# Kernel tuning notes

Measured on AMD Instinct MI355X. Metric: run time of the kernel, lower is better.

## Reference

```python
import jax, jax.numpy as jnp
import numpy as np

G = 32; N = G * G          # gridsize, num_nodes per graph
A = 16                      # n_agents
B = 32                      # batch_size
E = 4096                    # edges per graph (~4-neighbor grid)
F_IN = 16                   # input_dim
H = 64                      # hidden_dim
L = 3                       # n_graph_layers
MID = F_IN + L * H          # 208
CAT = 2 * MID + H           # 480
MIN_VAL = -1e8


def _layer_norm(x, g, b, eps=1e-5):
    m = x.mean(-1, keepdims=True)
    v = x.var(-1, keepdims=True)
    return (x - m) * jax.lax.rsqrt(v + eps) * g + b


def setup_inputs() -> dict:
    key = jax.random.key(0)
    ks = jax.random.split(key, 16)
    inp = {}
    inp["graph_nodes"] = jax.random.normal(ks[0], (B, N, F_IN), jnp.float32)
    inp["graph_edge_links"] = jax.random.randint(ks[1], (B, 2, E), 0, N)
    inp["agent_locations"] = jax.random.randint(ks[2], (B, A), 0, N)
    inp["mask"] = jax.random.bernoulli(ks[3], 0.5, (B, A * N))
    inp["dist_matrix"] = jax.random.uniform(ks[4], (N, N), jnp.float32)
    dims = [F_IN] + [H] * L
    k = 5
    for l in range(L):
        inp[f"conv{l}_W"] = jax.random.normal(ks[k], (dims[l], H), jnp.float32) * 0.05
        inp[f"conv{l}_b"] = jnp.zeros((H,), jnp.float32)
        inp[f"conv{l}_g"] = jnp.ones((H,), jnp.float32)
        inp[f"conv{l}_beta"] = jnp.zeros((H,), jnp.float32)
        k += 1
    inp["edges_W"] = jax.random.normal(ks[k], (1, H), jnp.float32) * 0.05
    inp["edges_b"] = jnp.zeros((H,), jnp.float32)
    inp["actor1_W"] = jax.random.normal(ks[k + 1], (CAT, MID), jnp.float32) * 0.05
    inp["actor1_b"] = jnp.zeros((MID,), jnp.float32)
    inp["bn_g"] = jnp.ones((MID,), jnp.float32)
    inp["bn_b"] = jnp.zeros((MID,), jnp.float32)
    inp["actor2_W"] = jax.random.normal(ks[k + 2], (MID, 1), jnp.float32) * 0.05
    inp["actor2_b"] = jnp.zeros((1,), jnp.float32)
    return inp


def reference(graph_nodes, graph_edge_links, agent_locations, mask, dist_matrix,
              conv0_W, conv0_b, conv0_g, conv0_beta,
              conv1_W, conv1_b, conv1_g, conv1_beta,
              conv2_W, conv2_b, conv2_g, conv2_beta,
              edges_W, edges_b, actor1_W, actor1_b, bn_g, bn_b,
              actor2_W, actor2_b):
    # --- batch graphs: offset node indices per graph (Batch.from_data_list) ---
    x = graph_nodes.reshape(B * N, F_IN)
    offs = (jnp.arange(B) * N)[:, None, None]
    ei = (graph_edge_links + offs).transpose(1, 0, 2).reshape(2, B * E)
    src, dst = ei[0], ei[1]

    conv_params = [(conv0_W, conv0_b, conv0_g, conv0_beta),
                   (conv1_W, conv1_b, conv1_g, conv1_beta),
                   (conv2_W, conv2_b, conv2_g, conv2_beta)]
    outs = [x]
    for W, bb, g, beta in conv_params:
        # GINConv with eps=-1: (1+eps)*x_i == 0, so out = mlp(sum_j x_j)
        agg = jax.ops.segment_sum(x[src], dst, num_segments=B * N)
        x = jax.nn.relu(_layer_norm(agg @ W + bb, g, beta))  # mlp relu; outer .relu() idempotent
        outs.append(x)
    xc = jnp.concatenate(outs, axis=1).reshape(B, N, MID)

    # --- all-pairs (agent, node) feature build ---
    a = jnp.take_along_axis(xc, agent_locations[:, :, None], axis=1)  # [B, A, MID]
    a = jnp.repeat(a, N, axis=1)                                      # [B, A*N, MID]
    bfeat = jnp.tile(xc, (1, A, 1))                                   # [B, A*N, MID]
    c = dist_matrix[agent_locations].reshape(B, A * N, 1)             # [B, A*N, 1]
    c = c @ edges_W + edges_b                                         # [B, A*N, H]
    h = jnp.concatenate([a, bfeat, c], axis=2).reshape(-1, CAT)

    h = h @ actor1_W + actor1_b
    mu = h.mean(0)
    var = h.var(0)
    h = (h - mu) * jax.lax.rsqrt(var + 1e-5) * bn_g + bn_b  # BatchNorm1d, training stats
    h = jax.nn.relu(h)
    logits = (h @ actor2_W + actor2_b).reshape(B, A * N)
    logits = jnp.where(mask, logits, MIN_VAL)
    return jax.nn.softmax(logits, axis=1)
```

## Files before the change

kernel.cpp:

```cpp
#include <hip/hip_runtime.h>
#include <cstddef>

#define B_    32
#define N_    1024
#define E_    4096
#define A_    16
#define FIN_  16
#define H_    64
#define MID_  208
#define NODES (B_ * N_)
#define NEDGE (B_ * E_)
#define ROWS  (B_ * A_ * N_)
#define AN_   (A_ * N_)

__device__ __forceinline__ float readlane_f(float v, int l) {
  return __uint_as_float(__builtin_amdgcn_readlane(__float_as_uint(v), l));
}

__global__ __launch_bounds__(256) void k_front(const int* __restrict__ el,
                                               const float* __restrict__ dist,
                                               const int* __restrict__ loc,
                                               const float* __restrict__ W1,
                                               const float* __restrict__ eW,
                                               const float* __restrict__ eb,
                                               const float* __restrict__ b1,
                                               int* __restrict__ rowptr,
                                               int* __restrict__ counts,
                                               int* __restrict__ ssrc,
                                               float* __restrict__ d1row,
                                               float* __restrict__ c2row,
                                               float* __restrict__ e1,
                                               float* __restrict__ cu,
                                               float* __restrict__ base) {
  __shared__ int cnt[1024];
  __shared__ int cur[1024];
  __shared__ int part[256];
  __shared__ int loc_s[16];
  int blk = blockIdx.x, t = threadIdx.x;
  if (blk < 32) {
    int b = blk;
    for (int i = t; i < 1024; i += 256) cnt[i] = 0;
    __syncthreads();
    const int* srcp = el + b * (2 * E_);
    const int* dstp = srcp + E_;
    for (int i = t; i < E_; i += 256) atomicAdd(&cnt[dstp[i]], 1);
    __syncthreads();
    int4 c4 = *(const int4*)&cnt[t * 4];
    int s = c4.x + c4.y + c4.z + c4.w;
    part[t] = s;
    __syncthreads();
    for (int off = 1; off < 256; off <<= 1) {
      int v = (t >= off) ? part[t - off] : 0;
      __syncthreads();
      part[t] += v;
      __syncthreads();
    }
    int prev = ((t == 0) ? 0 : part[t - 1]) + b * E_;
    int p0 = prev, p1 = p0 + c4.x, p2 = p1 + c4.y, p3 = p2 + c4.z;
    *(int4*)&rowptr[b * 1024 + t * 4] = make_int4(p0, p1, p2, p3);
    *(int4*)&counts[b * 1024 + t * 4] = c4;
    cur[t * 4 + 0] = p0;
    cur[t * 4 + 1] = p1;
    cur[t * 4 + 2] = p2;
    cur[t * 4 + 3] = p3;
    __syncthreads();
    for (int i = t; i < E_; i += 256) {
      int dl = dstp[i];
      int sl = srcp[i];
      int pos = atomicAdd(&cur[dl], 1);
      ssrc[pos] = b * N_ + sl;
    }
  } else if (blk < 288) {
    int lane = t & 63, w = t >> 6;
    int r = (blk - 32) * 4 + w;
    const float* dr = dist + (size_t)r * N_;
    float s = 0.f, c2 = 0.f;
#pragma unroll
    for (int k = 0; k < 16; k++) {
      float v = dr[lane + 64 * k];
      s += v;
      c2 = fmaf(v, v, c2);
    }
#pragma unroll
    for (int o = 32; o > 0; o >>= 1) { s += __shfl_xor(s, o); c2 += __shfl_xor(c2, o); }
    if (lane == 0) { d1row[r] = s; c2row[r] = c2; }
  } else if (blk < 320) {
    int b = blk - 288;
    if (t < 16) loc_s[t] = loc[b * 16 + t];
    __syncthreads();
    float e4[4] = {0.f, 0.f, 0.f, 0.f};
    for (int a = 0; a < 16; a++) {
      const float* dr = dist + (size_t)loc_s[a] * N_;
#pragma unroll
      for (int k = 0; k < 4; k++) e4[k] += dr[t + 256 * k];
    }
#pragma unroll
    for (int k = 0; k < 4; k++) e1[b * N_ + t + 256 * k] = e4[k];
  } else {
    int j = t;
    if (j < MID_) {
      float c = 0.f, bs = 0.f;
      for (int k = 0; k < H_; k++) {
        float w = W1[(2 * MID_ + k) * MID_ + j];
        c = fmaf(eW[k], w, c);
        bs = fmaf(eb[k], w, bs);
      }
      cu[j] = c;
      base[j] = bs + b1[j];
    }
  }
}

template <int FINT, bool COPYIN>
__global__ __launch_bounds__(256) void k_layer(const float* __restrict__ xin, int xstride, int in_off,
                                               float* __restrict__ xc, int out_off,
                                               const int* __restrict__ rowptr,
                                               const int* __restrict__ counts,
                                               const int* __restrict__ ssrc,
                                               const float* __restrict__ W,
                                               const float* __restrict__ bias,
                                               const float* __restrict__ g,
                                               const float* __restrict__ beta) {
  int t = threadIdx.x, lane = t & 63, w = t >> 6;
  float Wcol[FINT];
#pragma unroll
  for (int f = 0; f < FINT; f++) Wcol[f] = W[f * 64 + lane];
  float bv = bias[lane], gv = g[lane], bev = beta[lane];
  constexpr int CH = 64 / FINT;
  int f = lane & (FINT - 1);
  int ch = (FINT == 64) ? 0 : (lane >> 4);
  int nbase = (blockIdx.x * 4 + w) * 4;

  float agg[4];
#pragma unroll
  for (int nn = 0; nn < 4; nn++) {
    int node = nbase + nn;
    int r0 = rowptr[node];
    int deg = counts[node];
    float a0 = 0.f, a1 = 0.f, a2 = 0.f, a3 = 0.f;
    int e = ch;
    for (; e + 3 * CH < deg; e += 4 * CH) {
      int s0 = ssrc[r0 + e];
      int s1 = ssrc[r0 + e + CH];
      int s2 = ssrc[r0 + e + 2 * CH];
      int s3 = ssrc[r0 + e + 3 * CH];
      a0 += xin[(size_t)s0 * xstride + in_off + f];
      a1 += xin[(size_t)s1 * xstride + in_off + f];
      a2 += xin[(size_t)s2 * xstride + in_off + f];
      a3 += xin[(size_t)s3 * xstride + in_off + f];
    }
    for (; e < deg; e += CH) {
      int s = ssrc[r0 + e];
      a0 += xin[(size_t)s * xstride + in_off + f];
    }
    agg[nn] = (a0 + a1) + (a2 + a3);
  }

#pragma unroll
  for (int nn = 0; nn < 4; nn++) {
    int node = nbase + nn;
    float aggf = agg[nn];
    float y0 = bv, y1 = 0.f, y2 = 0.f, y3 = 0.f;
#pragma unroll
    for (int l = 0; l < 64; l += 4) {
      y0 = fmaf(readlane_f(aggf, l + 0), Wcol[(l + 0) & (FINT - 1)], y0);
      y1 = fmaf(readlane_f(aggf, l + 1), Wcol[(l + 1) & (FINT - 1)], y1);
      y2 = fmaf(readlane_f(aggf, l + 2), Wcol[(l + 2) & (FINT - 1)], y2);
      y3 = fmaf(readlane_f(aggf, l + 3), Wcol[(l + 3) & (FINT - 1)], y3);
    }
    float y = (y0 + y1) + (y2 + y3);
    float m = y;
#pragma unroll
    for (int o = 32; o > 0; o >>= 1) m += __shfl_xor(m, o);
    m *= (1.f / 64.f);
    float d = y - m;
    float vv = d * d;
#pragma unroll
    for (int o = 32; o > 0; o >>= 1) vv += __shfl_xor(vv, o);
    vv *= (1.f / 64.f);
    float outv = fmaxf(d * rsqrtf(vv + 1e-5f) * gv + bev, 0.f);
    xc[(size_t)node * MID_ + out_off + lane] = outv;
    if (COPYIN) {
      if (lane < FIN_) xc[(size_t)node * MID_ + lane] = xin[(size_t)node * FIN_ + lane];
    }
  }
}

template <int NR>
__device__ __forceinline__ void gemm_sc(const float* __restrict__ xc,
                                        const float* __restrict__ W1,
                                        int row0w, int j0, float acc[NR][4]) {
  const float* Bbase = W1 + (size_t)MID_ * MID_;
  const float* Arow = xc + (size_t)row0w * MID_;
#pragma unroll
  for (int r = 0; r < NR; r++)
#pragma unroll
    for (int q = 0; q < 4; q++) acc[r][q] = 0.f;

#pragma unroll 2
  for (int c = 0; c < 52; c++) {
    int k = c * 4;
    float4 a[NR];
    const float* ap = Arow + k;
#pragma unroll
    for (int r = 0; r < NR; r++) a[r] = *(const float4*)(ap + r * MID_);
#pragma unroll
    for (int q = 0; q < 4; q++) {
      float4 bq = *(const float4*)(Bbase + (size_t)(k + q) * MID_ + j0);
#pragma unroll
      for (int r = 0; r < NR; r++) {
        float ar = (q == 0) ? a[r].x : (q == 1) ? a[r].y : (q == 2) ? a[r].z : a[r].w;
        acc[r][0] = fmaf(ar, bq.x, acc[r][0]);
        acc[r][1] = fmaf(ar, bq.y, acc[r][1]);
        acc[r][2] = fmaf(ar, bq.z, acc[r][2]);
        acc[r][3] = fmaf(ar, bq.w, acc[r][3]);
      }
    }
  }
}

#define TSTR 105
__global__ __launch_bounds__(256) void k_p1(const float* __restrict__ xc,
                                            const float* __restrict__ W1,
                                            const float* __restrict__ e1,
                                            const int* __restrict__ loc,
                                            float* __restrict__ SBp,
                                            float* __restrict__ pBT,
                                            float* __restrict__ pA) {
  __shared__ float red[4 * 624];
  __shared__ float accS[32 * TSTR];
  __shared__ float xr[MID_];
  int t = threadIdx.x, lane = t & 63;
  int w = __builtin_amdgcn_readfirstlane(t >> 6);
  int blk = blockIdx.x;
  if (blk < 1024) {
    int row0 = blk * 32;
    int row0w = row0 + w * 8;
    int j0 = lane * 4;
    float acc[8][4];
    gemm_sc<8>(xc, W1, row0w, j0, acc);
    const float* ep = e1 + row0w;
    float4 e0 = *(const float4*)(ep);
    float4 e4 = *(const float4*)(ep + 4);
    float ev[8] = {e0.x, e0.y, e0.z, e0.w, e4.x, e4.y, e4.z, e4.w};
    if (j0 < MID_) {
      float s1[4] = {0, 0, 0, 0}, s2[4] = {0, 0, 0, 0}, se[4] = {0, 0, 0, 0};
#pragma unroll
      for (int r = 0; r < 8; r++) {
#pragma unroll
        for (int q = 0; q < 4; q++) {
          float v = acc[r][q];
          s1[q] += v;
          s2[q] = fmaf(v, v, s2[q]);
          se[q] = fmaf(v, ev[r], se[q]);
        }
      }
#pragma unroll
      for (int q = 0; q < 4; q++) {
        red[w * 624 + j0 + q] = s1[q];
        red[w * 624 + 208 + j0 + q] = s2[q];
        red[w * 624 + 416 + j0 + q] = se[q];
      }
    }
    __syncthreads();
    for (int idx = t; idx < 624; idx += 256) {
      SBp[(size_t)blk * 624 + idx] =
          (red[idx] + red[624 + idx]) + (red[1248 + idx] + red[1872 + idx]);
    }
#pragma unroll
    for (int half = 0; half < 2; half++) {
      int lo = half * 104;
      __syncthreads();
      if (j0 >= lo && j0 < lo + 104) {
        int jc = j0 - lo;
#pragma unroll
        for (int r = 0; r < 8; r++) {
          int ba = (w * 8 + r) * TSTR + jc;
          accS[ba + 0] = acc[r][0];
          accS[ba + 1] = acc[r][1];
          accS[ba + 2] = acc[r][2];
          accS[ba + 3] = acc[r][3];
        }
      }
      __syncthreads();
      int jb = lo + w * 26;
      if (lane < 32) {
#pragma unroll 2
        for (int jj = 0; jj < 26; jj++) {
          int j = jb + jj;
          pBT[(size_t)j * NODES + row0 + lane] = accS[lane * TSTR + (j - lo)];
        }
      }
    }
  } else {
    int ab = blk - 1024;
    int b = ab >> 4;
    int node = b * N_ + loc[ab];
    if (t < MID_) xr[t] = xc[(size_t)node * MID_ + t];
    __syncthreads();
    if (t < MID_) {
      float acc = 0.f;
      for (int i = 0; i < MID_; i++) acc = fmaf(xr[i], W1[i * MID_ + t], acc);
      pA[ab * MID_ + t] = acc;
    }
  }
}

__global__ __launch_bounds__(256) void k_fin(const float* __restrict__ SBp,
                                             const float* __restrict__ pA,
                                             const float* __restrict__ cu,
                                             const float* __restrict__ base,
                                             const float* __restrict__ d1row,
                                             const float* __restrict__ c2row,
                                             const int* __restrict__ loc,
                                             const float* __restrict__ bng,
                                             const float* __restrict__ bnb,
                                             const float* __restrict__ W2,
                                             float* __restrict__ vaT,
                                             float* __restrict__ wpack4) {
  __shared__ float utmp[1536 + 192];
  __shared__ float redm[4];
  __shared__ float reds[4];
  __shared__ float bcast[2];
  int t = threadIdx.x, lane = t & 63, w = t >> 6;
  int j = blockIdx.x;
  float cuj = cu[j], bj = base[j];
  int bb = t >> 3, ii = t & 7;
  float q1 = 0, q2 = 0, q3 = 0, t1 = 0, t2 = 0, t3 = 0;
#pragma unroll
  for (int i = ii * 4; i < ii * 4 + 4; i++) {
    const float* sp = SBp + (size_t)(bb * 32 + i) * 624;
    q1 += sp[j];
    q2 += sp[208 + j];
    q3 += sp[416 + j];
  }
#pragma unroll
  for (int a = ii * 2; a < ii * 2 + 2; a++) {
    int r = bb * 16 + a;
    float pa = pA[r * MID_ + j] + bj;
    t1 += pa;
    t2 = fmaf(pa, pa, t2);
    t3 = fmaf(pa, d1row[loc[r]], t3);
  }
  utmp[0 * 256 + t] = q1;
  utmp[1 * 256 + t] = q2;
  utmp[2 * 256 + t] = q3;
  utmp[3 * 256 + t] = t1;
  utmp[4 * 256 + t] = t2;
  utmp[5 * 256 + t] = t3;
  float p1 = 0.f, p2 = 0.f;
#pragma unroll
  for (int r = t * 2; r < t * 2 + 2; r++) {
    int l = loc[r];
    p1 += d1row[l];
    p2 += c2row[l];
  }
#pragma unroll
  for (int o = 32; o > 0; o >>= 1) { p1 += __shfl_xor(p1, o); p2 += __shfl_xor(p2, o); }
  if (lane == 0) { redm[w] = p1; reds[w] = p2; }
  __syncthreads();
  if (t < 192) {
    int s = t >> 5, b32 = t & 31;
    float ssum = 0.f;
#pragma unroll
    for (int i = 0; i < 8; i++) ssum += utmp[s * 256 + b32 * 8 + i];
    utmp[1536 + s * 32 + b32] = ssum;
  }
  __syncthreads();
  if (t == 0) {
    float Sc1 = (redm[0] + redm[1]) + (redm[2] + redm[3]);
    float Sc2 = (reds[0] + reds[1]) + (reds[2] + reds[3]);
    double T1 = 0, T2 = 0, T3 = 0, cross = 0, sp1 = 0, sp2 = 0, spe = 0;
    for (int b = 0; b < 32; b++) {
      float sq1 = utmp[1536 + 0 * 32 + b];
      float sq2 = utmp[1536 + 1 * 32 + b];
      float sq3 = utmp[1536 + 2 * 32 + b];
      float pt1 = utmp[1536 + 3 * 32 + b];
      float pt2 = utmp[1536 + 4 * 32 + b];
      float pt3 = utmp[1536 + 5 * 32 + b];
      T1 += pt1; T2 += pt2; T3 += pt3;
      cross += (double)pt1 * sq1;
      sp1 += sq1; sp2 += sq2; spe += sq3;
    }
    double s1 = 1024.0 * T1 + 16.0 * sp1 + (double)cuj * Sc1;
    double s2 = 1024.0 * T2 + 16.0 * sp2 + (double)cuj * cuj * Sc2 +
                2.0 * (cross + (double)cuj * (T3 + spe));
    double mu = s1 * (1.0 / (double)ROWS);
    double var = s2 * (1.0 / (double)ROWS) - mu * mu;
    float sc = (float)(1.0 / sqrt(var + 1e-5)) * bng[j];
    float sh = bnb[j] - (float)mu * sc;
    bcast[0] = sc;
    bcast[1] = sh;
    wpack4[4 * j + 0] = sc;
    wpack4[4 * j + 1] = cuj * sc;
    wpack4[4 * j + 2] = W2[j];
    wpack4[4 * j + 3] = 0.f;
  }
  __syncthreads();
  float sc = bcast[0], sh = bcast[1];
#pragma unroll
  for (int r = t * 2; r < t * 2 + 2; r++) {
    int b = r >> 4, a = r & 15;
    float pa = pA[r * MID_ + j] + bj;
    vaT[((size_t)b * MID_ + j) * 16 + a] = pa * sc + sh;
  }
}

__global__ __launch_bounds__(256) void k_logits(const float* __restrict__ pBT,
                                                const float* __restrict__ vaT,
                                                const float* __restrict__ wpack4,
                                                const float* __restrict__ dist,
                                                const int* __restrict__ loc,
                                                const int* __restrict__ mask,
                                                const float* __restrict__ b2,
                                                float* __restrict__ lg,
                                                float2* __restrict__ Psm) {
  __shared__ float accL[4][8][64];
  __shared__ int loc_s[16];
  __shared__ float redm[4];
  __shared__ float reds[4];
  int t = threadIdx.x, lane = t & 63;
  int w = __builtin_amdgcn_readfirstlane(t >> 6);
  int b = blockIdx.y, nt = blockIdx.x;
  int n0 = nt * 64;
  if (t < 16) loc_s[t] = loc[b * 16 + t];
  __syncthreads();
  float c[16];
#pragma unroll
  for (int a = 0; a < 16; a++) c[a] = dist[(size_t)loc_s[a] * N_ + n0 + lane];
  float acc16[16];
#pragma unroll
  for (int a = 0; a < 16; a++) acc16[a] = 0.f;
  const float4* wp = (const float4*)wpack4;
  int ng = b * N_ + n0 + lane;
  int jb = w * 52;
#pragma unroll 4
  for (int jj = 0; jj < 52; jj++) {
    int j = jb + jj;
    float pbv = pBT[(size_t)j * NODES + ng];
    float4 wv = wp[j];
    float pbs = pbv * wv.x;
    const float* va = vaT + ((size_t)b * MID_ + j) * 16;
#pragma unroll
    for (int a = 0; a < 16; a++) {
      float h = fmaf(c[a], wv.y, va[a] + pbs);
      h = fmaxf(h, 0.f);
      acc16[a] = fmaf(h, wv.z, acc16[a]);
    }
  }

  float b2v = b2[0];
  float sv[4];
  int ois[4];
  unsigned mk = 0;
#pragma unroll
  for (int half = 0; half < 2; half++) {
#pragma unroll
    for (int a8 = 0; a8 < 8; a8++) accL[t >> 6][a8][lane] = acc16[half * 8 + a8];
    __syncthreads();
#pragma unroll
    for (int p = 0; p < 2; p++) {
      int idx = p * 256 + t;
      int a8 = idx >> 6, nn = idx & 63;
      float s = (accL[0][a8][nn] + accL[1][a8][nn]) +
                (accL[2][a8][nn] + accL[3][a8][nn]) + b2v;
      int a = half * 8 + a8;
      int oi = b * AN_ + a * N_ + n0 + nn;
      int iv = half * 2 + p;
      bool m_ = mask[oi] != 0;
      sv[iv] = m_ ? s : -1e8f;
      ois[iv] = oi;
      mk |= (m_ ? 1u : 0u) << iv;
    }
    __syncthreads();
  }

  float mx = fmaxf(fmaxf(sv[0], sv[1]), fmaxf(sv[2], sv[3]));
#pragma unroll
  for (int o = 32; o > 0; o >>= 1) mx = fmaxf(mx, __shfl_xor(mx, o));
  if (lane == 0) redm[t >> 6] = mx;
  __syncthreads();
  mx = fmaxf(fmaxf(redm[0], redm[1]), fmaxf(redm[2], redm[3]));
  float ssum = 0.f;
#pragma unroll
  for (int iv = 0; iv < 4; iv++) {
    float pv = ((mk >> iv) & 1u) ? expf(sv[iv] - mx) : 0.f;
    lg[ois[iv]] = pv;
    ssum += pv;
  }
#pragma unroll
  for (int o = 32; o > 0; o >>= 1) ssum += __shfl_xor(ssum, o);
  if (lane == 0) reds[t >> 6] = ssum;
  __syncthreads();
  if (t == 0) Psm[b * 16 + nt] = make_float2(mx, (reds[0] + reds[1]) + (reds[2] + reds[3]));
}

__global__ __launch_bounds__(256) void k_sm2(const float* __restrict__ lg,
                                             const float2* __restrict__ P,
                                             float* __restrict__ out) {
  __shared__ float scs[16];
  int b = blockIdx.y, x = blockIdx.x, t = threadIdx.x;
  float M = -3.0e38f;
  float2 pr[16];
#pragma unroll
  for (int k = 0; k < 16; k++) {
    pr[k] = P[b * 16 + k];
    M = fmaxf(M, pr[k].x);
  }
  float S = 0.f;
#pragma unroll
  for (int k = 0; k < 16; k++) S += pr[k].y * expf(pr[k].x - M);
  float inv = 1.0f / S;
  if (t < 16) scs[t] = expf(pr[t].x - M) * inv;
  __syncthreads();
  const float* lb = lg + b * AN_ + x * 2048;
  float* ob = out + b * AN_ + x * 2048;
#pragma unroll
  for (int k = 0; k < 8; k++) {
    int i = t + 256 * k;
    int n = (x * 2048 + i) & 1023;
    ob[i] = lb[i] * scs[n >> 6];
  }
}

extern "C" void kernel_launch(void* const* d_in, const int* in_sizes, int n_in,
                              void* d_out, int out_size, void* d_ws, size_t ws_size,
                              hipStream_t stream) {
  const float* gn = (const float*)d_in[0];
  const int* el = (const int*)d_in[1];
  const int* loc = (const int*)d_in[2];
  const int* mask = (const int*)d_in[3];
  const float* dist = (const float*)d_in[4];
  const float* c0W = (const float*)d_in[5];
  const float* c0b = (const float*)d_in[6];
  const float* c0g = (const float*)d_in[7];
  const float* c0be = (const float*)d_in[8];
  const float* c1W = (const float*)d_in[9];
  const float* c1b = (const float*)d_in[10];
  const float* c1g = (const float*)d_in[11];
  const float* c1be = (const float*)d_in[12];
  const float* c2W = (const float*)d_in[13];
  const float* c2b = (const float*)d_in[14];
  const float* c2g = (const float*)d_in[15];
  const float* c2be = (const float*)d_in[16];
  const float* eW = (const float*)d_in[17];
  const float* eb = (const float*)d_in[18];
  const float* W1 = (const float*)d_in[19];
  const float* b1 = (const float*)d_in[20];
  const float* bng = (const float*)d_in[21];
  const float* bnb = (const float*)d_in[22];
  const float* W2 = (const float*)d_in[23];
  const float* b2 = (const float*)d_in[24];
  float* out = (float*)d_out;

  char* p = (char*)d_ws;
  auto alloc = [&](size_t bytes) {
    char* r = p;
    p += (bytes + 255) & ~(size_t)255;
    return r;
  };
  int* counts = (int*)alloc((size_t)NODES * 4);
  int* rowptr = (int*)alloc((size_t)NODES * 4);
  int* ssrc = (int*)alloc((size_t)NEDGE * 4);
  float* xc = (float*)alloc((size_t)NODES * MID_ * 4);
  float* pBT = (float*)alloc((size_t)NODES * MID_ * 4);
  float* pA = (float*)alloc((size_t)512 * MID_ * 4);
  float* cu = (float*)alloc(256 * 4);
  float* base = (float*)alloc(256 * 4);
  float* d1row = (float*)alloc((size_t)N_ * 4);
  float* c2row = (float*)alloc((size_t)N_ * 4);
  float* e1 = (float*)alloc((size_t)B_ * N_ * 4);
  float* SBp = (float*)alloc((size_t)1024 * 624 * 4);
  float* vaT = (float*)alloc((size_t)B_ * MID_ * 16 * 4);
  float* wpack4 = (float*)alloc((size_t)MID_ * 4 * 4);
  float* lg = (float*)alloc((size_t)ROWS * 4);
  float2* Psm = (float2*)alloc((size_t)B_ * 16 * 8);

  k_front<<<321, 256, 0, stream>>>(el, dist, loc, W1, eW, eb, b1,
                                   rowptr, counts, ssrc, d1row, c2row, e1, cu, base);

  k_layer<16, true><<<2048, 256, 0, stream>>>(gn, FIN_, 0, xc, 16, rowptr, counts, ssrc, c0W, c0b, c0g, c0be);
  k_layer<64, false><<<2048, 256, 0, stream>>>(xc, MID_, 16, xc, 80, rowptr, counts, ssrc, c1W, c1b, c1g, c1be);
  k_layer<64, false><<<2048, 256, 0, stream>>>(xc, MID_, 80, xc, 144, rowptr, counts, ssrc, c2W, c2b, c2g, c2be);

  k_p1<<<1536, 256, 0, stream>>>(xc, W1, e1, loc, SBp, pBT, pA);
  k_fin<<<208, 256, 0, stream>>>(SBp, pA, cu, base, d1row, c2row, loc, bng, bnb, W2, vaT, wpack4);

  k_logits<<<dim3(16, 32), 256, 0, stream>>>(pBT, vaT, wpack4, dist, loc, mask, b2, lg, Psm);
  k_sm2<<<dim3(8, 32), 256, 0, stream>>>(lg, Psm, out);
}
```

Before: 268.0 us.

## Halve k_p1 row tile to 16 rows and alias shared buffers for occupancy

The projection kernel k_p1 now processes 16 node rows per block instead of 32, so it launches twice as many GEMM blocks and each thread keeps a 4x4 accumulator instead of 8x4. Its three shared arrays are merged into one aliased buffer, which shrinks LDS per block. The transposed pBT store is remapped so all 64 lanes write (16 nodes by 4 columns). The partial-sum buffer SBp doubles in size and k_fin reduces 8 partials per thread instead of 4. The intent is more resident waves and better latency hiding, at the cost of less W1 reuse per block and more partial-sum traffic.

After: 281.6 us. 5.1% more time.

```diff
diff --git a/kernel.cpp b/kernel.cpp
--- a/kernel.cpp
+++ b/kernel.cpp
@@ -227,26 +227,23 @@
                                             float* __restrict__ SBp,
                                             float* __restrict__ pBT,
                                             float* __restrict__ pA) {
-  __shared__ float red[4 * 624];
-  __shared__ float accS[32 * TSTR];
-  __shared__ float xr[MID_];
+  __shared__ float smem[2496];
   int t = threadIdx.x, lane = t & 63;
   int w = __builtin_amdgcn_readfirstlane(t >> 6);
   int blk = blockIdx.x;
-  if (blk < 1024) {
-    int row0 = blk * 32;
-    int row0w = row0 + w * 8;
+  if (blk < 2048) {
+    int row0 = blk * 16;
+    int row0w = row0 + w * 4;
     int j0 = lane * 4;
-    float acc[8][4];
-    gemm_sc<8>(xc, W1, row0w, j0, acc);
+    float acc[4][4];
+    gemm_sc<4>(xc, W1, row0w, j0, acc);
     const float* ep = e1 + row0w;
     float4 e0 = *(const float4*)(ep);
-    float4 e4 = *(const float4*)(ep + 4);
-    float ev[8] = {e0.x, e0.y, e0.z, e0.w, e4.x, e4.y, e4.z, e4.w};
+    float ev[4] = {e0.x, e0.y, e0.z, e0.w};
     if (j0 < MID_) {
       float s1[4] = {0, 0, 0, 0}, s2[4] = {0, 0, 0, 0}, se[4] = {0, 0, 0, 0};
 #pragma unroll
-      for (int r = 0; r < 8; r++) {
+      for (int r = 0; r < 4; r++) {
 #pragma unroll
         for (int q = 0; q < 4; q++) {
           float v = acc[r][q];
@@ -257,15 +254,15 @@
       }
 #pragma unroll
       for (int q = 0; q < 4; q++) {
-        red[w * 624 + j0 + q] = s1[q];
-        red[w * 624 + 208 + j0 + q] = s2[q];
-        red[w * 624 + 416 + j0 + q] = se[q];
+        smem[w * 624 + j0 + q] = s1[q];
+        smem[w * 624 + 208 + j0 + q] = s2[q];
+        smem[w * 624 + 416 + j0 + q] = se[q];
       }
     }
     __syncthreads();
     for (int idx = t; idx < 624; idx += 256) {
       SBp[(size_t)blk * 624 + idx] =
-          (red[idx] + red[624 + idx]) + (red[1248 + idx] + red[1872 + idx]);
+          (smem[idx] + smem[624 + idx]) + (smem[1248 + idx] + smem[1872 + idx]);
     }
 #pragma unroll
     for (int half = 0; half < 2; half++) {
@@ -274,28 +271,31 @@
       if (j0 >= lo && j0 < lo + 104) {
         int jc = j0 - lo;
 #pragma unroll
-        for (int r = 0; r < 8; r++) {
-          int ba = (w * 8 + r) * TSTR + jc;
-          accS[ba + 0] = acc[r][0];
-          accS[ba + 1] = acc[r][1];
-          accS[ba + 2] = acc[r][2];
-          accS[ba + 3] = acc[r][3];
+        for (int r = 0; r < 4; r++) {
+          int ba = (w * 4 + r) * TSTR + jc;
+          smem[ba + 0] = acc[r][0];
+          smem[ba + 1] = acc[r][1];
+          smem[ba + 2] = acc[r][2];
+          smem[ba + 3] = acc[r][3];
         }
       }
       __syncthreads();
       int jb = lo + w * 26;
-      if (lane < 32) {
-#pragma unroll 2
-        for (int jj = 0; jj < 26; jj++) {
-          int j = jb + jj;
-          pBT[(size_t)j * NODES + row0 + lane] = accS[lane * TSTR + (j - lo)];
+      int node = lane & 15;
+      int jo = lane >> 4;
+      for (int jj = 0; jj < 28; jj += 4) {
+        int jr = jj + jo;
+        if (jr < 26) {
+          int j = jb + jr;
+          pBT[(size_t)j * NODES + row0 + node] = smem[node * TSTR + (j - lo)];
         }
       }
     }
   } else {
-    int ab = blk - 1024;
+    int ab = blk - 2048;
     int b = ab >> 4;
     int node = b * N_ + loc[ab];
+    float* xr = smem;
     if (t < MID_) xr[t] = xc[(size_t)node * MID_ + t];
     __syncthreads();
     if (t < MID_) {
@@ -328,8 +328,8 @@
   int bb = t >> 3, ii = t & 7;
   float q1 = 0, q2 = 0, q3 = 0, t1 = 0, t2 = 0, t3 = 0;
 #pragma unroll
-  for (int i = ii * 4; i < ii * 4 + 4; i++) {
-    const float* sp = SBp + (size_t)(bb * 32 + i) * 624;
+  for (int i = ii * 8; i < ii * 8 + 8; i++) {
+    const float* sp = SBp + (size_t)(bb * 64 + i) * 624;
     q1 += sp[j];
     q2 += sp[208 + j];
     q3 += sp[416 + j];
@@ -570,7 +570,7 @@
   float* d1row = (float*)alloc((size_t)N_ * 4);
   float* c2row = (float*)alloc((size_t)N_ * 4);
   float* e1 = (float*)alloc((size_t)B_ * N_ * 4);
-  float* SBp = (float*)alloc((size_t)1024 * 624 * 4);
+  float* SBp = (float*)alloc((size_t)2048 * 624 * 4);
   float* vaT = (float*)alloc((size_t)B_ * MID_ * 16 * 4);
   float* wpack4 = (float*)alloc((size_t)MID_ * 4 * 4);
   float* lg = (float*)alloc((size_t)ROWS * 4);
@@ -583,7 +583,7 @@
   k_layer<64, false><<<2048, 256, 0, stream>>>(xc, MID_, 16, xc, 80, rowptr, counts, ssrc, c1W, c1b, c1g, c1be);
   k_layer<64, false><<<2048, 256, 0, stream>>>(xc, MID_, 80, xc, 144, rowptr, counts, ssrc, c2W, c2b, c2g, c2be);
 
-  k_p1<<<1536, 256, 0, stream>>>(xc, W1, e1, loc, SBp, pBT, pA);
+  k_p1<<<2560, 256, 0, stream>>>(xc, W1, e1, loc, SBp, pBT, pA);
   k_fin<<<208, 256, 0, stream>>>(SBp, pA, cu, base, d1row, c2row, loc, bng, bnb, W2, vaT, wpack4);
 
   k_logits<<<dim3(16, 32), 256, 0, stream>>>(pBT, vaT, wpack4, dist, loc, mask, b2, lg, Psm);
```
